# Kernel tuning notes

Measured on AMD Instinct MI355X. Metric: run time of the kernel, lower is better.

Reference implementation:

```python
import jax, jax.numpy as jnp
import numpy as np

TEXT_VOCAB = 32000
CB = 1024          # audio_codebook_size
NCB = 8            # audio_num_codebooks
H = 2048           # hidden_size
NH = 16            # attention heads
NKV = 4            # kv heads (GQA)
HD = H // NH       # head dim = 128
FF = 8192          # ffn intermediate
L = 2              # num layers
EPS = 1e-5


def rmsnorm(x, w):
    v = jnp.mean(x * x, axis=-1, keepdims=True)
    return x * jax.lax.rsqrt(v + EPS) * w


def rope(x, pos):
    # x: [B,S,h,d], rotate-half style RoPE
    d = x.shape[-1]
    inv = 1.0 / (10000.0 ** (jnp.arange(0, d, 2, dtype=jnp.float32) / d))
    ang = pos[:, None] * inv[None, :]                 # [S, d/2]
    cos = jnp.cos(ang)[None, :, None, :]
    sin = jnp.sin(ang)[None, :, None, :]
    x1, x2 = x[..., : d // 2], x[..., d // 2 :]
    return jnp.concatenate([x1 * cos - x2 * sin, x2 * cos + x1 * sin], axis=-1)


def attention(x, wq, wk, wv, wo, pos, mask_bias):
    B, S, _ = x.shape
    q = (x @ wq).reshape(B, S, NH, HD)
    k = (x @ wk).reshape(B, S, NKV, HD)
    v = (x @ wv).reshape(B, S, NKV, HD)
    q = rope(q, pos)
    k = rope(k, pos)
    k = jnp.repeat(k, NH // NKV, axis=2)
    v = jnp.repeat(v, NH // NKV, axis=2)
    scores = jnp.einsum('bqhd,bkhd->bhqk', q, k) / np.float32(np.sqrt(HD))
    p = jax.nn.softmax(scores + mask_bias, axis=-1)
    o = jnp.einsum('bhqk,bkhd->bqhd', p, v).reshape(B, S, NH * HD)
    return o @ wo


def mlp(x, wfc, wproj):
    return jax.nn.silu(x @ wfc) @ wproj


def setup_inputs() -> dict:
    key = jax.random.key(0)
    ks = jax.random.split(key, 20)
    s = 0.02
    inp = {
        'input_ids': jax.random.randint(ks[0], (1, 2048), 0, TEXT_VOCAB + CB, dtype=jnp.int64 if jax.config.jax_enable_x64 else jnp.int32),
        'vocab_emb': jax.random.normal(ks[1], (TEXT_VOCAB, H), jnp.float32) * s,
        'audio_emb': jax.random.normal(ks[2], (NCB * CB, H), jnp.float32) * s,
        'ln_in_text': jnp.ones((L, H), jnp.float32),
        'ln_in_audio': jnp.ones((L, H), jnp.float32),
        'ln_post_text': jnp.ones((L, H), jnp.float32),
        'ln_post_audio': jnp.ones((L, H), jnp.float32),
        'wq': jax.random.normal(ks[3], (L, H, NH * HD), jnp.float32) * s,
        'wk': jax.random.normal(ks[4], (L, H, NKV * HD), jnp.float32) * s,
        'wv': jax.random.normal(ks[5], (L, H, NKV * HD), jnp.float32) * s,
        'wo': jax.random.normal(ks[6], (L, NH * HD, H), jnp.float32) * s,
        'wfc_text': jax.random.normal(ks[7], (L, H, FF), jnp.float32) * s,
        'wproj_text': jax.random.normal(ks[8], (L, FF, H), jnp.float32) * s,
        'wfc_audio': jax.random.normal(ks[9], (L, H, FF), jnp.float32) * s,
        'wproj_audio': jax.random.normal(ks[10], (L, FF, H), jnp.float32) * s,
        'ln_f': jnp.ones((H,), jnp.float32),
    }
    return inp


def reference(input_ids, vocab_emb, audio_emb, ln_in_text, ln_in_audio,
              ln_post_text, ln_post_audio, wq, wk, wv, wo,
              wfc_text, wproj_text, wfc_audio, wproj_audio, ln_f):
    B, S = input_ids.shape
    amask = input_ids > TEXT_VOCAB - 1                      # [B,S] audio-token mask
    text_tok = jnp.where(amask, TEXT_VOCAB - 1, input_ids)
    text_e = vocab_emb[text_tok]                            # [B,S,H]
    audio_tok = jnp.where(amask, input_ids - TEXT_VOCAB, 0)
    shift = (jnp.arange(NCB) * CB)[:, None, None]           # [NCB,1,1]
    audio_e = audio_emb[audio_tok[None] + shift].sum(0)     # sum over codebooks -> [B,S,H]
    h = jnp.where(amask[..., None], audio_e, text_e)

    pos = jnp.arange(S, dtype=jnp.float32)
    causal = jnp.tril(jnp.ones((S, S), bool))
    mask_bias = jnp.where(causal, 0.0, -1e9).astype(jnp.float32)[None, None]
    m = amask[..., None]

    for i in range(L):
        res = h
        hn = jnp.where(m, rmsnorm(h, ln_in_audio[i]), rmsnorm(h, ln_in_text[i]))
        h = res + attention(hn, wq[i], wk[i], wv[i], wo[i], pos, mask_bias)
        res = h
        t = mlp(rmsnorm(h, ln_post_text[i]), wfc_text[i], wproj_text[i])
        a = mlp(rmsnorm(h, ln_post_audio[i]), wfc_audio[i], wproj_audio[i])
        h = res + jnp.where(m, a, t)

    return rmsnorm(h, ln_f)
```

## Files before the change

kernel.cpp:

```cpp
#include <hip/hip_runtime.h>
#include <hip/hip_bf16.h>
#include <math.h>

#define S_LEN 2048
#define HID   2048

typedef __bf16 bf16x8 __attribute__((ext_vector_type(8)));
typedef float  f32x4  __attribute__((ext_vector_type(4)));

__device__ __forceinline__ unsigned short f2b(float x) {
  __hip_bfloat16 h = __float2bfloat16(x);
  return __builtin_bit_cast(unsigned short, h);
}

__device__ __forceinline__ float block_sum_256(float v) {
  __shared__ float red[4];
  #pragma unroll
  for (int o = 32; o > 0; o >>= 1) v += __shfl_down(v, o, 64);
  if ((threadIdx.x & 63) == 0) red[threadIdx.x >> 6] = v;
  __syncthreads();
  v = red[0] + red[1] + red[2] + red[3];
  __syncthreads();
  return v;
}

__global__ __launch_bounds__(256) void embed_kernel(
    const int* __restrict__ ids, const float* __restrict__ vemb,
    const float* __restrict__ aemb, float* __restrict__ h, int* __restrict__ amask) {
  const int s = blockIdx.x;
  const int id = ids[s];
  const bool am = id > 31999;
  if (threadIdx.x == 0) amask[s] = am ? 1 : 0;
  const int d0 = threadIdx.x * 8;
  float out[8];
  if (am) {
    const int at = id - 32000;
    #pragma unroll
    for (int u = 0; u < 8; u++) out[u] = 0.f;
    for (int cb = 0; cb < 8; cb++) {
      const float* src = aemb + (long)(at + cb * 1024) * HID + d0;
      #pragma unroll
      for (int u = 0; u < 8; u++) out[u] += src[u];
    }
  } else {
    const float* src = vemb + (long)id * HID + d0;
    #pragma unroll
    for (int u = 0; u < 8; u++) out[u] = src[u];
  }
  float* dst = h + (long)s * HID + d0;
  #pragma unroll
  for (int u = 0; u < 8; u++) dst[u] = out[u];
}

__global__ __launch_bounds__(256) void partition_rows(
    const int* __restrict__ ids, int* __restrict__ apos, int* __restrict__ cnt) {
  __shared__ int ca[256];
  __shared__ int sc[257];
  const int t = threadIdx.x;
  int m[8], loc = 0;
  #pragma unroll
  for (int i = 0; i < 8; i++) { m[i] = ids[t * 8 + i] > 31999 ? 1 : 0; loc += m[i]; }
  ca[t] = loc;
  __syncthreads();
  if (t == 0) {
    int run = 0;
    for (int i = 0; i < 256; i++) { sc[i] = run; run += ca[i]; }
    sc[256] = run;
  }
  __syncthreads();
  int off = sc[t];
  #pragma unroll
  for (int i = 0; i < 8; i++) {
    const int s = t * 8 + i;
    if (m[i]) { apos[s] = off; off++; }
    else apos[s] = -1;
  }
  if (t == 0) { cnt[0] = sc[256]; cnt[1] = (sc[256] + 127) & ~127; }
}

__global__ void init_ctrs(int* c) { c[threadIdx.x] = 0; }

__global__ __launch_bounds__(256) void init_stats(float* __restrict__ stm, float* __restrict__ stl) {
  const int i = blockIdx.x * 256 + threadIdx.x;
  stm[i] = -1e30f;
  stl[i] = 0.f;
}

__global__ __launch_bounds__(256) void transposew(
    const float* __restrict__ W, int ldw, unsigned short* __restrict__ Wt, int K, int N) {
  __shared__ float t[64][65];
  const int k0 = blockIdx.y * 64, n0 = blockIdx.x * 64;
  const int q = threadIdx.x & 15;
  const int r0 = threadIdx.x >> 4;
  #pragma unroll
  for (int i = 0; i < 4; i++) {
    const int row = r0 + i * 16;
    const float4 v = *(const float4*)(W + (long)(k0 + row) * ldw + n0 + q * 4);
    t[row][q * 4 + 0] = v.x; t[row][q * 4 + 1] = v.y;
    t[row][q * 4 + 2] = v.z; t[row][q * 4 + 3] = v.w;
  }
  __syncthreads();
  #pragma unroll
  for (int i = 0; i < 4; i++) {
    const int n = r0 + i * 16;
    ushort4 o;
    o.x = f2b(t[q * 4 + 0][n]); o.y = f2b(t[q * 4 + 1][n]);
    o.z = f2b(t[q * 4 + 2][n]); o.w = f2b(t[q * 4 + 3][n]);
    *(ushort4*)(Wt + (long)(n0 + n) * K + k0 + q * 4) = o;
  }
}

__global__ __launch_bounds__(256) void transpose_b16(
    const unsigned short* __restrict__ V, unsigned short* __restrict__ Vt) {
  __shared__ unsigned short t[64][72];
  const int s0 = blockIdx.y * 64, d0 = blockIdx.x * 64;
  const int q = threadIdx.x & 15;
  const int r0 = threadIdx.x >> 4;
  #pragma unroll
  for (int i = 0; i < 4; i++) {
    const int row = r0 + i * 16;
    const ushort4 v = *(const ushort4*)(V + (long)(s0 + row) * 512 + d0 + q * 4);
    t[row][q * 4 + 0] = v.x; t[row][q * 4 + 1] = v.y;
    t[row][q * 4 + 2] = v.z; t[row][q * 4 + 3] = v.w;
  }
  __syncthreads();
  #pragma unroll
  for (int i = 0; i < 4; i++) {
    const int d = r0 + i * 16;
    ushort4 o;
    o.x = t[q * 4 + 0][d]; o.y = t[q * 4 + 1][d];
    o.z = t[q * 4 + 2][d]; o.w = t[q * 4 + 3][d];
    *(ushort4*)(Vt + (long)(d0 + d) * 2048 + s0 + q * 4) = o;
  }
}

__global__ __launch_bounds__(256) void rope_table(float* __restrict__ c, float* __restrict__ s_) {
  const int i = blockIdx.x * 256 + threadIdx.x;
  const int pos = i >> 6, j = i & 63;
  const float inv = powf(10000.f, -(float)(2 * j) * (1.f / 128.f));
  const float ang = (float)pos * inv;
  c[i] = cosf(ang);
  s_[i] = sinf(ang);
}

__global__ __launch_bounds__(256) void rmsnorm_sel(
    const float* __restrict__ x, const int* __restrict__ amask,
    const float* __restrict__ wt, const float* __restrict__ wa, unsigned short* __restrict__ out) {
  const long s = blockIdx.x;
  const float* xr = x + s * HID;
  const int d0 = threadIdx.x * 8;
  float v[8], ss = 0.f;
  #pragma unroll
  for (int u = 0; u < 8; u++) { v[u] = xr[d0 + u]; ss += v[u] * v[u]; }
  ss = block_sum_256(ss) * (1.f / HID);
  const float rr = rsqrtf(ss + 1e-5f);
  const float* w = amask[s] ? wa : wt;
  #pragma unroll
  for (int u = 0; u < 8; u++) out[s * HID + d0 + u] = f2b(v[u] * rr * w[d0 + u]);
}

__global__ __launch_bounds__(256) void rmsnorm_post(
    const float* __restrict__ x, const int* __restrict__ apos,
    const float* __restrict__ wt, const float* __restrict__ wa,
    unsigned short* __restrict__ hnt, unsigned short* __restrict__ hna_g) {
  const long s = blockIdx.x;
  const float* xr = x + s * HID;
  const int d0 = threadIdx.x * 8;
  float v[8], ss = 0.f;
  #pragma unroll
  for (int u = 0; u < 8; u++) { v[u] = xr[d0 + u]; ss += v[u] * v[u]; }
  ss = block_sum_256(ss) * (1.f / HID);
  const float rr = rsqrtf(ss + 1e-5f);
  const int ap = apos[s];
  #pragma unroll
  for (int u = 0; u < 8; u++) {
    const float xn = v[u] * rr;
    hnt[s * HID + d0 + u] = f2b(xn * wt[d0 + u]);
    if (ap >= 0) hna_g[(long)ap * HID + d0 + u] = f2b(xn * wa[d0 + u]);
  }
}

__global__ __launch_bounds__(256) void rmsnorm_final(
    const float* __restrict__ x, const float* __restrict__ w, float* __restrict__ out) {
  const long s = blockIdx.x;
  const float* xr = x + s * HID;
  const int d0 = threadIdx.x * 8;
  float v[8], ss = 0.f;
  #pragma unroll
  for (int u = 0; u < 8; u++) { v[u] = xr[d0 + u]; ss += v[u] * v[u]; }
  ss = block_sum_256(ss) * (1.f / HID);
  const float rr = rsqrtf(ss + 1e-5f);
  #pragma unroll
  for (int u = 0; u < 8; u++) out[s * HID + d0 + u] = v[u] * rr * w[d0 + u];
}

__device__ __forceinline__ void gload16(const void* g, void* l) {
  __builtin_amdgcn_global_load_lds((const __attribute__((address_space(1))) void*)g,
                                   (__attribute__((address_space(3))) void*)l, 16, 0, 0);
}

#define ABAR() do { __builtin_amdgcn_s_barrier(); \
  asm volatile("" ::: "memory"); __builtin_amdgcn_sched_barrier(0); } while (0)

__global__ __launch_bounds__(512, 1) void attn_flash(
    const unsigned short* __restrict__ qb, const unsigned short* __restrict__ kb,
    const unsigned short* __restrict__ vt, float* __restrict__ opart,
    float* __restrict__ stm, float* __restrict__ stl,
    int* __restrict__ ctr, float iscale) {
  __shared__ __align__(16) unsigned short Kb[2][2][128][64];
  __shared__ __align__(16) unsigned short Vb[2][128][64];
  __shared__ __align__(16) unsigned short Pb[8][16][144];
  __shared__ int s_item;
  const int tid = threadIdx.x;
  const int lane = tid & 63;
  const int w = tid >> 6;
  const int lr = lane & 15;
  const int kg = lane >> 4;
  const int trow = tid >> 3;
  const int tc = tid & 7;

  for (;;) {
    if (tid == 0) s_item = atomicAdd(ctr, 1);
    __syncthreads();
    const int item = s_item;
    __syncthreads();
    if (item >= 512) break;
    const int qq = 15 - (item >> 5);
    const int h = item & 15;
    const int cch = (item >> 4) & 1;
    const int kvh = h >> 2;
    const int bm = qq * 128;
    const int nt = qq + 1;
    const int tmid = (nt + 1) >> 1;
    const int t0 = cch ? tmid : 0;
    const int t1 = cch ? nt : tmid;
    if (t0 >= t1) continue;

    bf16x8 af_q[4];
    {
      const unsigned short* qr = qb + (long)(bm + w * 16 + lr) * 2048 + h * 128 + kg * 8;
      #pragma unroll
      for (int c = 0; c < 4; c++) af_q[c] = *(const bf16x8*)(qr + c * 32);
    }
    float m[4], l[4];
    #pragma unroll
    for (int r = 0; r < 4; r++) { m[r] = -1e30f; l[r] = 0.f; }
    f32x4 acc_o[8];
    #pragma unroll
    for (int nf = 0; nf < 8; nf++) acc_o[nf] = (f32x4){0.f, 0.f, 0.f, 0.f};

    auto stageK = [&](int buf, int t) {
      const int kv0 = t * 128;
      #pragma unroll
      for (int hh2 = 0; hh2 < 2; hh2++)
        #pragma unroll
        for (int rr = 0; rr < 2; rr++) {
          const int row = trow + rr * 64;
          gload16(kb + (long)(kv0 + row) * 512 + kvh * 128 + hh2 * 64 + ((tc ^ (row & 7)) * 8),
                  &Kb[buf][hh2][row][tc * 8]);
        }
    };
    auto stageV = [&](int t) {
      const int kv0 = t * 128;
      #pragma unroll
      for (int hh2 = 0; hh2 < 2; hh2++)
        #pragma unroll
        for (int rr = 0; rr < 2; rr++) {
          const int row = trow + rr * 64;
          gload16(vt + (long)(kvh * 128 + row) * 2048 + kv0 + hh2 * 64 + ((tc ^ (row & 7)) * 8),
                  &Vb[hh2][row][tc * 8]);
        }
    };

    stageK(t0 & 1, t0);
    for (int t = t0; t < t1; t++) {
      const bool hn = (t + 1) < t1;
      stageV(t);
      if (hn) stageK((t + 1) & 1, t + 1);
      if (hn) { asm volatile("s_waitcnt vmcnt(8)" ::: "memory"); }
      else    { asm volatile("s_waitcnt vmcnt(4)" ::: "memory"); }
      ABAR();
      f32x4 acc[8];
      #pragma unroll
      for (int nf = 0; nf < 8; nf++) acc[nf] = (f32x4){0.f, 0.f, 0.f, 0.f};
      #pragma unroll
      for (int c = 0; c < 4; c++) {
        #pragma unroll
        for (int nf = 0; nf < 8; nf++) {
          const int row = nf * 16 + lr;
          bf16x8 bk = *(const bf16x8*)(&Kb[t & 1][c >> 1][row][(((c & 1) * 4 + kg) ^ (row & 7)) * 8]);
          acc[nf] = __builtin_amdgcn_mfma_f32_16x16x32_bf16(af_q[c], bk, acc[nf], 0, 0, 0);
        }
      }
      const bool diag = (t == nt - 1);
      #pragma unroll
      for (int r = 0; r < 4; r++) {
        const int rowg = bm + w * 16 + kg * 4 + r;
        float sv[8], tmax = -1e30f;
        #pragma unroll
        for (int nf = 0; nf < 8; nf++) {
          float s = acc[nf][r] * iscale;
          const int colg = t * 128 + nf * 16 + lr;
          if (diag && colg > rowg) s = -1e30f;
          sv[nf] = s;
          tmax = fmaxf(tmax, s);
        }
        #pragma unroll
        for (int o = 1; o < 16; o <<= 1) tmax = fmaxf(tmax, __shfl_xor(tmax, o, 64));
        const float mn = fmaxf(m[r], tmax);
        const float scal = __expf(m[r] - mn);
        float psum = 0.f;
        #pragma unroll
        for (int nf = 0; nf < 8; nf++) {
          const float pe = __expf(sv[nf] - mn);
          psum += pe;
          Pb[w][kg * 4 + r][nf * 16 + lr] = f2b(pe);
        }
        #pragma unroll
        for (int o = 1; o < 16; o <<= 1) psum += __shfl_xor(psum, o, 64);
        l[r] = l[r] * scal + psum;
        m[r] = mn;
        #pragma unroll
        for (int nf = 0; nf < 8; nf++) acc_o[nf][r] *= scal;
      }
      asm volatile("s_waitcnt lgkmcnt(0)" ::: "memory");
      __builtin_amdgcn_sched_barrier(0);
      if (hn) { asm volatile("s_waitcnt vmcnt(4)" ::: "memory"); }
      else    { asm volatile("s_waitcnt vmcnt(0)" ::: "memory"); }
      ABAR();
      #pragma unroll
      for (int c = 0; c < 4; c++) {
        bf16x8 ap = *(const bf16x8*)(&Pb[w][lr][c * 32 + kg * 8]);
        #pragma unroll
        for (int nf = 0; nf < 8; nf++) {
          const int row = nf * 16 + lr;
          bf16x8 bv = *(const bf16x8*)(&Vb[c >> 1][row][(((c & 1) * 4 + kg) ^ (row & 7)) * 8]);
          acc_o[nf] = __builtin_amdgcn_mfma_f32_16x16x32_bf16(ap, bv, acc_o[nf], 0, 0, 0);
        }
      }
      ABAR();
    }
    float* op = opart + (long)cch * 4194304;
    #pragma unroll
    for (int nf = 0; nf < 8; nf++)
      #pragma unroll
      for (int r = 0; r < 4; r++)
        op[(long)(bm + w * 16 + kg * 4 + r) * 2048 + h * 128 + nf * 16 + lr] = acc_o[nf][r];
    if (lr == 0) {
      #pragma unroll
      for (int r = 0; r < 4; r++) {
        const int row = bm + w * 16 + kg * 4 + r;
        stm[(cch * 16 + h) * 2048 + row] = m[r];
        stl[(cch * 16 + h) * 2048 + row] = l[r];
      }
    }
    __syncthreads();
  }
}

__global__ __launch_bounds__(256) void o_merge2(
    const float* __restrict__ op, const float* __restrict__ stm,
    const float* __restrict__ stl, unsigned short* __restrict__ o) {
  const int i = blockIdx.x * 256 + threadIdx.x;
  const int s = i >> 11, c = i & 2047, h = c >> 7;
  const int si = h * 2048 + s;
  const float m1 = stm[si], l1 = stl[si];
  const float m2 = stm[32768 + si], l2 = stl[32768 + si];
  const float M = fmaxf(m1, m2);
  const float w1 = __expf(m1 - M), w2 = __expf(m2 - M);
  const float denom = l1 * w1 + l2 * w2;
  o[i] = f2b((op[i] * w1 + op[i + 4194304] * w2) / denom);
}

__global__ __launch_bounds__(256) void mlp_reduce(
    const float* __restrict__ pt, const float* __restrict__ pa,
    const int* __restrict__ apos, float* __restrict__ h) {
  const int i = blockIdx.x * 256 + threadIdx.x;
  const int r = i >> 11, c = i & 2047;
  const long Z = (long)1 << 22;
  const int ap = apos[r];
  float val;
  if (ap < 0) {
    val = pt[i] + pt[i + Z] + pt[i + 2 * Z] + pt[i + 3 * Z];
  } else {
    const long b = (long)ap * 2048 + c;
    val = 0.f;
    #pragma unroll
    for (int k = 0; k < 8; k++) val += pa[k * Z + b];
  }
  h[i] += val;
}

template <int BM, int BN, int EPI>
__global__ __launch_bounds__(512) void gemm2(
    const unsigned short* __restrict__ A, int lda, long sAz,
    const unsigned short* __restrict__ Bt, int ldb, long sBz,
    void* __restrict__ Cv, int ldc, long sCz, long sCx, int K, float scale,
    const int* __restrict__ ecnt, int kspl,
    const float* __restrict__ rc, const float* __restrict__ rs,
    unsigned short* __restrict__ kbo, unsigned short* __restrict__ vbo) {
  constexpr int MF = BM / 32;
  constexpr int NF = BN / 64;
  __shared__ __align__(16) unsigned short smem[2 * (BM + BN) * 64];
  const int tid = threadIdx.x;
  const int lane = tid & 63;
  const int wave = tid >> 6;
  const int bm = blockIdx.y * BM;
  const int z = blockIdx.z;
  int bn, kbeg, nt;
  if constexpr (EPI == 7) {
    bn = blockIdx.x * BN;
    kbeg = z * kspl;
    nt = kspl / 64;
  } else {
    bn = blockIdx.x * BN;
    kbeg = 0;
    nt = K / 64;
  }
  if constexpr (EPI == 2 || EPI == 7) {
    if (bm >= ecnt[1]) return;
  }
  A += sAz * z;
  Bt += sBz * z;
  const int wm = (wave >> 2) * (BM / 2);
  const int wn = (wave & 3) * (BN / 4);
  const int lr = lane & 15;
  const int kg = lane >> 4;
  const int swx = lr & 7;
  const int trow = tid >> 3;
  const int tc = tid & 7;
  const long aoff = (long)(bm + trow) * lda + ((tc ^ (trow & 7)) * 8);
  const long boff = (long)(bn + trow) * ldb + ((tc ^ (trow & 7)) * 8);

  f32x4 acc[MF][NF];
  #pragma unroll
  for (int m = 0; m < MF; m++)
    #pragma unroll
    for (int n = 0; n < NF; n++) acc[m][n] = (f32x4){0.f, 0.f, 0.f, 0.f};

  auto stage = [&](int buf, int k0) {
    unsigned short* sA = &smem[(size_t)buf * (BM + BN) * 64];
    #pragma unroll
    for (int r = 0; r < BM / 64; r++)
      gload16(A + aoff + (long)r * 64 * lda + k0, sA + r * 4096 + tid * 8);
    unsigned short* sB = sA + BM * 64;
    #pragma unroll
    for (int r = 0; r < BN / 64; r++)
      gload16(Bt + boff + (long)r * 64 * ldb + k0, sB + r * 4096 + tid * 8);
  };
  auto compute = [&](int buf) {
    const unsigned short* sA = &smem[(size_t)buf * (BM + BN) * 64];
    const unsigned short* sB = sA + BM * 64;
    #pragma unroll
    for (int ks = 0; ks < 2; ks++) {
      bf16x8 af[MF], bv[NF];
      #pragma unroll
      for (int m = 0; m < MF; m++) {
        const int row = wm + m * 16 + lr;
        af[m] = *(const bf16x8*)(sA + row * 64 + (((ks * 4 + kg) ^ swx) * 8));
      }
      #pragma unroll
      for (int n = 0; n < NF; n++) {
        const int row = wn + n * 16 + lr;
        bv[n] = *(const bf16x8*)(sB + row * 64 + (((ks * 4 + kg) ^ swx) * 8));
      }
      #pragma unroll
      for (int m = 0; m < MF; m++)
        #pragma unroll
        for (int n = 0; n < NF; n++)
          acc[m][n] = __builtin_amdgcn_mfma_f32_16x16x32_bf16(af[m], bv[n], acc[m][n], 0, 0, 0);
    }
  };

  if (nt > 0) {
    stage(0, kbeg);
    asm volatile("s_waitcnt vmcnt(0)" ::: "memory");
    __syncthreads();
    int cur = 0;
    for (int t = 0; t < nt; t++) {
      if (t + 1 < nt) stage(cur ^ 1, kbeg + (t + 1) * 64);
      compute(cur);
      asm volatile("s_waitcnt vmcnt(0)" ::: "memory");
      __syncthreads();
      cur ^= 1;
    }
  }

  if constexpr (EPI == 8) {
    if (bn >= 2560) {
      #pragma unroll
      for (int m = 0; m < MF; m++)
        #pragma unroll
        for (int n = 0; n < NF; n++)
          #pragma unroll
          for (int r = 0; r < 4; r++) {
            const int grow = bm + wm + m * 16 + kg * 4 + r;
            const int gcol = bn + wn + n * 16 + lr;
            vbo[(long)grow * 512 + (gcol - 2560)] = f2b(acc[m][n][r]);
          }
    } else {
      float* Cl = (float*)smem;
      #pragma unroll
      for (int m = 0; m < MF; m++)
        #pragma unroll
        for (int n = 0; n < NF; n++)
          #pragma unroll
          for (int r = 0; r < 4; r++)
            Cl[(wm + m * 16 + kg * 4 + r) * 128 + wn + n * 16 + lr] = acc[m][n][r];
      __syncthreads();
      const int j = tid & 63;
      const int r2 = tid >> 6;
      #pragma unroll
      for (int it = 0; it < 16; it++) {
        const int row = r2 + it * 8;
        const int s = bm + row;
        const float c = rc[s * 64 + j], sn = rs[s * 64 + j];
        const float x1 = Cl[row * 128 + j], x2 = Cl[row * 128 + j + 64];
        const unsigned short o1 = f2b(x1 * c - x2 * sn);
        const unsigned short o2 = f2b(x2 * c + x1 * sn);
        if (bn < 2048) {
          unsigned short* qp = (unsigned short*)Cv + (long)s * 2048 + bn + j;
          qp[0] = o1; qp[64] = o2;
        } else {
          unsigned short* kp = kbo + (long)s * 512 + (bn - 2048) + j;
          kp[0] = o1; kp[64] = o2;
        }
      }
    }
    return;
  }

  #pragma unroll
  for (int m = 0; m < MF; m++) {
    #pragma unroll
    for (int n = 0; n < NF; n++) {
      #pragma unroll
      for (int r = 0; r < 4; r++) {
        const int grow = bm + wm + m * 16 + kg * 4 + r;
        const int gcol = bn + wn + n * 16 + lr;
        const long idx = (long)grow * ldc + gcol;
        float v = acc[m][n][r];
        if constexpr (EPI == 2) {
          ((unsigned short*)Cv)[idx] = f2b(v / (1.f + expf(-v)));
        } else if constexpr (EPI == 3) {
          ((float*)Cv)[idx] += v;
        } else if constexpr (EPI == 7) {
          ((float*)Cv)[(long)z * sCz + idx] = v;
        }
      }
    }
  }
}

template <int EPI>
__global__ __launch_bounds__(512, 1) void gemm8(
    const unsigned short* __restrict__ A0, const unsigned short* __restrict__ A1, int lda,
    const unsigned short* __restrict__ Bt, long sBz, int ldb,
    void* __restrict__ Cv, int ldc, long sCz, int K) {
  __shared__ __align__(16) unsigned short smem[2][4][8192];
  const int tid = threadIdx.x;
  const int lane = tid & 63;
  const int wave = tid >> 6;
  const int bm = blockIdx.y * 256;
  const int bn = blockIdx.x * 256;
  const int z = blockIdx.z;
  const unsigned short* Aq;
  const unsigned short* Bq;
  if constexpr (EPI == 10) {
    Aq = z ? A1 : A0;
    Bq = Bt + (long)z * sBz;
  } else {
    Aq = A0 + z * 2048;
    Bq = Bt + z * 2048;
  }
  const int nt = K / 64;
  const int trow = tid >> 3;
  const int tc = tid & 7;
  const int sws = (tc ^ (trow & 7)) * 8;
  const int lr = lane & 15;
  const int kg = lane >> 4;
  const int wr = (wave >> 2) * 64;
  const int wc = (wave & 3) * 32;

  f32x4 acc[2][2][4][2];
  #pragma unroll
  for (int mh = 0; mh < 2; mh++)
    #pragma unroll
    for (int nh = 0; nh < 2; nh++)
      #pragma unroll
      for (int mf = 0; mf < 4; mf++)
        #pragma unroll
        for (int nf = 0; nf < 2; nf++) acc[mh][nh][mf][nf] = (f32x4){0.f, 0.f, 0.f, 0.f};

  bf16x8 af[2][4], bv0[2][2], bv1[2][2];

  auto stageA = [&](int buf, int half, int k0) {
    const unsigned short* g = Aq + (long)(bm + half * 128 + trow) * lda + k0 + sws;
    unsigned short* l = &smem[buf][half][0] + tid * 8;
    gload16(g, l);
    gload16(g + (long)64 * lda, l + 4096);
  };
  auto stageB = [&](int buf, int half, int k0) {
    const unsigned short* g = Bq + (long)(bn + half * 128 + trow) * ldb + k0 + sws;
    unsigned short* l = &smem[buf][2 + half][0] + tid * 8;
    gload16(g, l);
    gload16(g + (long)64 * ldb, l + 4096);
  };

#define GSYNC(VM) \
  asm volatile("s_waitcnt vmcnt(" #VM ")" ::: "memory"); \
  __builtin_amdgcn_s_barrier(); \
  asm volatile("" ::: "memory"); \
  __builtin_amdgcn_sched_barrier(0)

#define RD_A(BUF, MH) do { \
    _Pragma("unroll") \
    for (int ks = 0; ks < 2; ++ks) { \
      _Pragma("unroll") \
      for (int mf = 0; mf < 4; ++mf) { \
        const int row = wr + mf * 16 + lr; \
        af[ks][mf] = *(const bf16x8*)(&smem[BUF][MH][0] + row * 64 + (((ks * 4 + kg) ^ (row & 7)) * 8)); \
      } \
    } \
  } while (0)

#define RD_B(BUF, NH, BV) do { \
    _Pragma("unroll") \
    for (int ks = 0; ks < 2; ++ks) { \
      _Pragma("unroll") \
      for (int nf = 0; nf < 2; ++nf) { \
        const int row = wc + nf * 16 + lr; \
        BV[ks][nf] = *(const bf16x8*)(&smem[BUF][2 + NH][0] + row * 64 + (((ks * 4 + kg) ^ (row & 7)) * 8)); \
      } \
    } \
  } while (0)

#define DO_MFMA(MH, NH, BV) do { \
    __builtin_amdgcn_s_setprio(1); \
    _Pragma("unroll") \
    for (int ks = 0; ks < 2; ++ks) \
      _Pragma("unroll") \
      for (int mf = 0; mf < 4; ++mf) \
        _Pragma("unroll") \
        for (int nf = 0; nf < 2; ++nf) \
          acc[MH][NH][mf][nf] = __builtin_amdgcn_mfma_f32_16x16x32_bf16( \
              af[ks][mf], BV[ks][nf], acc[MH][NH][mf][nf], 0, 0, 0); \
    __builtin_amdgcn_s_setprio(0); \
  } while (0)

  stageA(0, 0, 0); stageB(0, 0, 0); stageB(0, 1, 0); stageA(0, 1, 0);
  stageA(1, 0, 64); stageB(1, 0, 64); stageB(1, 1, 64);
  GSYNC(10);

  for (int t = 0; t <= nt - 3; ++t) {
    const int b = t & 1, nb = b ^ 1;
    const int k1 = (t + 1) << 6, k2 = (t + 2) << 6;
    RD_A(b, 0); RD_B(b, 0, bv0); stageA(nb, 1, k1); DO_MFMA(0, 0, bv0); GSYNC(10);
    RD_B(b, 1, bv1);             stageA(b, 0, k2);  DO_MFMA(0, 1, bv1); GSYNC(10);
    RD_A(b, 1);                  stageB(b, 0, k2);  DO_MFMA(1, 1, bv1); GSYNC(10);
                                 stageB(b, 1, k2);  DO_MFMA(1, 0, bv0); GSYNC(10);
  }
  {
    const int t = nt - 2;
    const int b = t & 1, nb = b ^ 1;
    const int k1 = (t + 1) << 6;
    RD_A(b, 0); RD_B(b, 0, bv0); stageA(nb, 1, k1); DO_MFMA(0, 0, bv0); GSYNC(10);
    RD_B(b, 1, bv1);                                DO_MFMA(0, 1, bv1); GSYNC(8);
    RD_A(b, 1);                                     DO_MFMA(1, 1, bv1); GSYNC(8);
                                                    DO_MFMA(1, 0, bv0); GSYNC(4);
  }
  {
    const int b = (nt - 1) & 1;
    RD_A(b, 0); RD_B(b, 0, bv0); DO_MFMA(0, 0, bv0); GSYNC(2);
    RD_B(b, 1, bv1);             DO_MFMA(0, 1, bv1); GSYNC(0);
    RD_A(b, 1);                  DO_MFMA(1, 1, bv1); GSYNC(0);
                                 DO_MFMA(1, 0, bv0);
  }
#undef DO_MFMA
#undef RD_B
#undef RD_A
#undef GSYNC

  #pragma unroll
  for (int mh = 0; mh < 2; mh++) {
    #pragma unroll
    for (int nh = 0; nh < 2; nh++) {
      #pragma unroll
      for (int mf = 0; mf < 4; mf++) {
        #pragma unroll
        for (int nf = 0; nf < 2; nf++) {
          #pragma unroll
          for (int r = 0; r < 4; r++) {
            const int grow = bm + mh * 128 + wr + mf * 16 + kg * 4 + r;
            const int gcol = bn + nh * 128 + wc + nf * 16 + lr;
            const long idx = (long)z * sCz + (long)grow * ldc + gcol;
            const float v = acc[mh][nh][mf][nf][r];
            if constexpr (EPI == 10) {
              ((unsigned short*)Cv)[idx] = f2b(v / (1.f + expf(-v)));
            } else {
              ((float*)Cv)[idx] = v;
            }
          }
        }
      }
    }
  }
}

__global__ __launch_bounds__(256) void fill_zero(float* p, long n) {
  const long i = (long)blockIdx.x * 256 + threadIdx.x;
  if (i < n) p[i] = 0.f;
}

extern "C" void kernel_launch(void* const* d_in, const int* in_sizes, int n_in,
                              void* d_out, int out_size, void* d_ws, size_t ws_size,
                              hipStream_t stream) {
  const int* ids = (const int*)d_in[0];
  const float* vocab_emb = (const float*)d_in[1];
  const float* audio_emb = (const float*)d_in[2];
  const float* ln_in_text = (const float*)d_in[3];
  const float* ln_in_audio = (const float*)d_in[4];
  const float* ln_post_text = (const float*)d_in[5];
  const float* ln_post_audio = (const float*)d_in[6];
  const float* wq = (const float*)d_in[7];
  const float* wk = (const float*)d_in[8];
  const float* wv = (const float*)d_in[9];
  const float* wo = (const float*)d_in[10];
  const float* wfc_t = (const float*)d_in[11];
  const float* wpj_t = (const float*)d_in[12];
  const float* wfc_a = (const float*)d_in[13];
  const float* wpj_a = (const float*)d_in[14];
  const float* ln_f = (const float*)d_in[15];

  size_t off = 0;
  auto alloc = [&](size_t bytes) -> void* {
    void* p = (char*)d_ws + off;
    off += (bytes + 255) & ~(size_t)255;
    return p;
  };
  const size_t LW = 77594624;
  unsigned short* wsT = (unsigned short*)alloc((size_t)2 * LW * 2);
  int* amask = (int*)alloc(S_LEN * 4);
  int* apos = (int*)alloc(S_LEN * 4);
  int* cnt = (int*)alloc(16);
  int* ctrs = (int*)alloc(16);
  float* ropec = (float*)alloc((size_t)S_LEN * 64 * 4);
  float* ropes = (float*)alloc((size_t)S_LEN * 64 * 4);
  float* h = (float*)alloc((size_t)S_LEN * HID * 4);
  unsigned short* hn = (unsigned short*)alloc((size_t)S_LEN * HID * 2);
  unsigned short* hnt = (unsigned short*)alloc((size_t)S_LEN * HID * 2);
  unsigned short* hna_g = (unsigned short*)alloc((size_t)S_LEN * HID * 2);
  unsigned short* qb = (unsigned short*)alloc((size_t)S_LEN * 2048 * 2);
  unsigned short* kb = (unsigned short*)alloc((size_t)S_LEN * 512 * 2);
  unsigned short* vb = (unsigned short*)alloc((size_t)S_LEN * 512 * 2);
  unsigned short* vt = (unsigned short*)alloc((size_t)512 * S_LEN * 2);
  unsigned short* o = (unsigned short*)alloc((size_t)S_LEN * 2048 * 2);
  float* stm = (float*)alloc((size_t)2 * 16 * 2048 * 4);
  float* stl = (float*)alloc((size_t)2 * 16 * 2048 * 4);
  char* big = (char*)alloc(268435456);
  float* opart = (float*)big;
  unsigned short* mlp_t = (unsigned short*)big;
  unsigned short* mlp_a = (unsigned short*)(big + 33554432);
  float* pt = (float*)(big + 67108864);
  float* pa = (float*)(big + 134217728);

  if (ws_size < off) {
    fill_zero<<<(out_size + 255) / 256, 256, 0, stream>>>((float*)d_out, out_size);
    return;
  }

  const size_t WO_ = 6291456, WFT = 10485760, WPT = 27262976, WFA = 44040192, WPA = 60817408;

  embed_kernel<<<S_LEN, 256, 0, stream>>>(ids, vocab_emb, audio_emb, h, amask);
  partition_rows<<<1, 256, 0, stream>>>(ids, apos, cnt);
  init_ctrs<<<1, 4, 0, stream>>>(ctrs);
  init_stats<<<256, 256, 0, stream>>>(stm, stl);
  rope_table<<<S_LEN * 64 / 256, 256, 0, stream>>>(ropec, ropes);

  for (int i = 0; i < 2; i++) {
    const size_t wb = (size_t)i * LW;
    transposew<<<dim3(32, 32), 256, 0, stream>>>(wq + (size_t)i * 2048 * 2048, 2048, wsT + wb, 2048, 2048);
    transposew<<<dim3(8, 32), 256, 0, stream>>>(wk + (size_t)i * 2048 * 512, 512, wsT + wb + 4194304, 2048, 512);
    transposew<<<dim3(8, 32), 256, 0, stream>>>(wv + (size_t)i * 2048 * 512, 512, wsT + wb + 5242880, 2048, 512);
    transposew<<<dim3(32, 32), 256, 0, stream>>>(wo + (size_t)i * 2048 * 2048, 2048, wsT + wb + WO_, 2048, 2048);
    transposew<<<dim3(128, 32), 256, 0, stream>>>(wfc_t + (size_t)i * 2048 * 8192, 8192, wsT + wb + WFT, 2048, 8192);
    transposew<<<dim3(32, 128), 256, 0, stream>>>(wpj_t + (size_t)i * 8192 * 2048, 2048, wsT + wb + WPT, 8192, 2048);
    transposew<<<dim3(128, 32), 256, 0, stream>>>(wfc_a + (size_t)i * 2048 * 8192, 8192, wsT + wb + WFA, 2048, 8192);
    transposew<<<dim3(32, 128), 256, 0, stream>>>(wpj_a + (size_t)i * 8192 * 2048, 2048, wsT + wb + WPA, 8192, 2048);
  }

  const float iscale = 0.08838834764831845f;
  for (int i = 0; i < 2; i++) {
    const size_t wb = (size_t)i * LW;
    rmsnorm_sel<<<S_LEN, 256, 0, stream>>>(h, amask, ln_in_text + i * HID, ln_in_audio + i * HID, hn);
    gemm2<128, 128, 8><<<dim3(24, 16, 1), 512, 0, stream>>>(hn, 2048, 0, wsT + wb, 2048, 0,
        qb, 2048, 0, 0, 2048, 1.f, nullptr, 0, ropec, ropes, kb, vb);
    transpose_b16<<<dim3(8, 32), 256, 0, stream>>>(vb, vt);
    attn_flash<<<256, 512, 0, stream>>>(qb, kb, vt, opart, stm, stl, ctrs + i, iscale);
    o_merge2<<<16384, 256, 0, stream>>>(opart, stm, stl, o);
    gemm2<128, 128, 3><<<dim3(16, 16, 1), 512, 0, stream>>>(o, 2048, 0, wsT + wb + WO_, 2048, 0,
        h, 2048, 0, 0, 2048, 1.f, nullptr, 0, nullptr, nullptr, nullptr, nullptr);
    rmsnorm_post<<<S_LEN, 256, 0, stream>>>(h, apos, ln_post_text + i * HID, ln_post_audio + i * HID, hnt, hna_g);
    gemm2<128, 128, 2><<<dim3(64, 16, 1), 512, 0, stream>>>(hna_g, 2048, 0, wsT + wb + WFA, 2048, 0,
        mlp_a, 8192, 0, 0, 2048, 1.f, cnt, 0, nullptr, nullptr, nullptr, nullptr);
    gemm8<10><<<dim3(32, 8, 1), 512, 0, stream>>>(hnt, hnt, 2048, wsT + wb + WFT, 0, 2048,
        mlp_t, 8192, 0, 2048);
    gemm2<128, 128, 7><<<dim3(16, 16, 8), 512, 0, stream>>>(mlp_a, 8192, 0, wsT + wb + WPA, 8192, 0,
        pa, 2048, (long)1 << 22, 0, 8192, 1.f, cnt, 1024, nullptr, nullptr, nullptr, nullptr);
    gemm8<11><<<dim3(8, 8, 4), 512, 0, stream>>>(mlp_t, mlp_t, 8192, wsT + wb + WPT, 0, 8192,
        pt, 2048, (long)1 << 22, 2048);
    mlp_reduce<<<16384, 256, 0, stream>>>(pt, pa, apos, h);
  }
  rmsnorm_final<<<S_LEN, 256, 0, stream>>>(h, ln_f, (float*)d_out);
}
```

Before: 986.4 us.

## Reschedule GEMM LDS reads with double A fragment registers and reordered staging

Adds a second A-fragment register set so both A halves can live in registers at once. LDS reads and global-to-LDS stage calls are interleaved in a new order, with B half-1 read up front and B half-0 re-read late, and vmcnt wait counts are adjusted to match. The aim is to overlap LDS reads with MFMA work and to free shared-memory buffers earlier. In exchange it uses more VGPRs, which may lower occupancy, and it risks wait-count or hazard mistakes in the tail iterations.

```diff
diff --git a/kernel.cpp b/kernel.cpp
--- a/kernel.cpp
+++ b/kernel.cpp
@@ -592,7 +592,7 @@
         #pragma unroll
         for (int nf = 0; nf < 2; nf++) acc[mh][nh][mf][nf] = (f32x4){0.f, 0.f, 0.f, 0.f};
 
-  bf16x8 af[2][4], bv0[2][2], bv1[2][2];
+  bf16x8 af[2][4], af2[2][4], bv0[2][2], bv1[2][2];
 
   auto stageA = [&](int buf, int half, int k0) {
     const unsigned short* g = Aq + (long)(bm + half * 128 + trow) * lda + k0 + sws;
@@ -613,29 +613,29 @@
   asm volatile("" ::: "memory"); \
   __builtin_amdgcn_sched_barrier(0)
 
-#define RD_A(BUF, MH) do { \
+#define RD_A(BUF, MH, DST) do { \
     _Pragma("unroll") \
     for (int ks = 0; ks < 2; ++ks) { \
       _Pragma("unroll") \
       for (int mf = 0; mf < 4; ++mf) { \
         const int row = wr + mf * 16 + lr; \
-        af[ks][mf] = *(const bf16x8*)(&smem[BUF][MH][0] + row * 64 + (((ks * 4 + kg) ^ (row & 7)) * 8)); \
+        DST[ks][mf] = *(const bf16x8*)(&smem[BUF][MH][0] + row * 64 + (((ks * 4 + kg) ^ (row & 7)) * 8)); \
       } \
     } \
   } while (0)
 
-#define RD_B(BUF, NH, BV) do { \
+#define RD_B(BUF, NH, DST) do { \
     _Pragma("unroll") \
     for (int ks = 0; ks < 2; ++ks) { \
       _Pragma("unroll") \
       for (int nf = 0; nf < 2; ++nf) { \
         const int row = wc + nf * 16 + lr; \
-        BV[ks][nf] = *(const bf16x8*)(&smem[BUF][2 + NH][0] + row * 64 + (((ks * 4 + kg) ^ (row & 7)) * 8)); \
+        DST[ks][nf] = *(const bf16x8*)(&smem[BUF][2 + NH][0] + row * 64 + (((ks * 4 + kg) ^ (row & 7)) * 8)); \
       } \
     } \
   } while (0)
 
-#define DO_MFMA(MH, NH, BV) do { \
+#define DO_MFMA(MH, NH, AF, BV) do { \
     __builtin_amdgcn_s_setprio(1); \
     _Pragma("unroll") \
     for (int ks = 0; ks < 2; ++ks) \
@@ -644,37 +644,42 @@
         _Pragma("unroll") \
         for (int nf = 0; nf < 2; ++nf) \
           acc[MH][NH][mf][nf] = __builtin_amdgcn_mfma_f32_16x16x32_bf16( \
-              af[ks][mf], BV[ks][nf], acc[MH][NH][mf][nf], 0, 0, 0); \
+              AF[ks][mf], BV[ks][nf], acc[MH][NH][mf][nf], 0, 0, 0); \
     __builtin_amdgcn_s_setprio(0); \
   } while (0)
 
   stageA(0, 0, 0); stageB(0, 0, 0); stageB(0, 1, 0); stageA(0, 1, 0);
-  stageA(1, 0, 64); stageB(1, 0, 64); stageB(1, 1, 64);
-  GSYNC(10);
+  stageA(1, 0, 64); stageB(1, 1, 64); stageB(1, 0, 64);
+  GSYNC(8);
 
   for (int t = 0; t <= nt - 3; ++t) {
     const int b = t & 1, nb = b ^ 1;
     const int k1 = (t + 1) << 6, k2 = (t + 2) << 6;
-    RD_A(b, 0); RD_B(b, 0, bv0); stageA(nb, 1, k1); DO_MFMA(0, 0, bv0); GSYNC(10);
-    RD_B(b, 1, bv1);             stageA(b, 0, k2);  DO_MFMA(0, 1, bv1); GSYNC(10);
-    RD_A(b, 1);                  stageB(b, 0, k2);  DO_MFMA(1, 1, bv1); GSYNC(10);
-                                 stageB(b, 1, k2);  DO_MFMA(1, 0, bv0); GSYNC(10);
+    RD_A(b, 0, af); RD_B(b, 0, bv0); RD_B(b, 1, bv1);
+    stageA(nb, 1, k1); DO_MFMA(0, 0, af, bv0); GSYNC(8);
+    RD_A(b, 1, af2);
+    stageA(b, 0, k2); DO_MFMA(0, 1, af, bv1); GSYNC(8);
+    stageB(b, 1, k2); DO_MFMA(1, 1, af2, bv1); GSYNC(8);
+    RD_B(b, 0, bv0);
+    stageB(b, 0, k2); DO_MFMA(1, 0, af2, bv0); GSYNC(8);
   }
   {
     const int t = nt - 2;
     const int b = t & 1, nb = b ^ 1;
     const int k1 = (t + 1) << 6;
-    RD_A(b, 0); RD_B(b, 0, bv0); stageA(nb, 1, k1); DO_MFMA(0, 0, bv0); GSYNC(10);
-    RD_B(b, 1, bv1);                                DO_MFMA(0, 1, bv1); GSYNC(8);
-    RD_A(b, 1);                                     DO_MFMA(1, 1, bv1); GSYNC(8);
-                                                    DO_MFMA(1, 0, bv0); GSYNC(4);
+    RD_A(b, 0, af); RD_B(b, 0, bv0); RD_B(b, 1, bv1);
+    stageA(nb, 1, k1); DO_MFMA(0, 0, af, bv0); GSYNC(8);
+    RD_A(b, 1, af2); DO_MFMA(0, 1, af, bv1); GSYNC(8);
+    DO_MFMA(1, 1, af2, bv1); GSYNC(8);
+    RD_B(b, 0, bv0); DO_MFMA(1, 0, af2, bv0); GSYNC(2);
   }
   {
     const int b = (nt - 1) & 1;
-    RD_A(b, 0); RD_B(b, 0, bv0); DO_MFMA(0, 0, bv0); GSYNC(2);
-    RD_B(b, 1, bv1);             DO_MFMA(0, 1, bv1); GSYNC(0);
-    RD_A(b, 1);                  DO_MFMA(1, 1, bv1); GSYNC(0);
-                                 DO_MFMA(1, 0, bv0);
+    RD_A(b, 0, af); RD_B(b, 0, bv0); RD_B(b, 1, bv1);
+    DO_MFMA(0, 0, af, bv0); GSYNC(0);
+    RD_A(b, 1, af2); DO_MFMA(0, 1, af, bv1);
+    DO_MFMA(1, 1, af2, bv1);
+    RD_B(b, 0, bv0); DO_MFMA(1, 0, af2, bv0);
   }
 #undef DO_MFMA
 #undef RD_B
```

After: 988.9 us. About the same (+0.3%).
